# Optimization experiments

Hardware: AMD Instinct MI355X
Metric: run time of the kernel (lower is better)

The kernel has to match this reference:

```python
import jax, jax.numpy as jnp
import numpy as np
import math

N_HEADS = 16
EMBED = 1024
D_HEAD = EMBED // N_HEADS
B, L = 2, 2048


def setup_inputs() -> dict:
    key = jax.random.key(0)
    k1, k2, k3, k4, k5 = jax.random.split(key, 5)
    s = 0.02
    return {
        "x": jax.random.normal(k1, (B, L, EMBED), dtype=jnp.float32),
        "w_qkv": jax.random.normal(k2, (3 * EMBED, EMBED), dtype=jnp.float32) * s,
        "b_qkv": jax.random.normal(k3, (3 * EMBED,), dtype=jnp.float32) * s,
        "w_out": jax.random.normal(k4, (EMBED, EMBED), dtype=jnp.float32) * s,
        "b_out": jax.random.normal(k5, (EMBED,), dtype=jnp.float32) * s,
        "mask": 1,
    }


def reference(x, w_qkv, b_qkv, w_out, b_out, mask):
    b, l, e = x.shape
    qkv = x @ w_qkv.T + b_qkv                      # (B, L, 3E)
    q, k, v = jnp.split(qkv, 3, axis=-1)
    # (B, L, H, d) -> (B, H, L, d)
    q = q.reshape(b, l, N_HEADS, D_HEAD).transpose(0, 2, 1, 3)
    k = k.reshape(b, l, N_HEADS, D_HEAD).transpose(0, 2, 1, 3)
    v = v.reshape(b, l, N_HEADS, D_HEAD).transpose(0, 2, 1, 3)
    # NOTE: faithful to source bug -- scores use V, not K
    scores = jnp.einsum("bhld,bhmd->bhlm", q, v) * (1.0 / math.sqrt(D_HEAD))
    if mask:
        causal = jnp.triu(jnp.ones((l, l), dtype=bool), k=1)  # (L, L)
        scores = jnp.where(causal, -jnp.inf, scores)
    attn = jax.nn.softmax(scores, axis=-1)          # (B, H, L, L)
    out = jnp.einsum("bhlm,bhmd->bhld", attn, v)    # (B, H, L, d)
    # NOTE: faithful to source bug -- transpose(1,2) result discarded,
    # so reshape straight from (B, H, L, d) to (B, L, E)
    out = out.reshape(b, l, e)
    return out @ w_out.T + b_out
```

## Files before the change

kernel.cpp:

```cpp
#include <hip/hip_runtime.h>
#include <math.h>

constexpr int Lc = 2048, Ec = 1024, Hc = 16, Dc = 64;

typedef __attribute__((ext_vector_type(8))) short bf16x8;
typedef __attribute__((ext_vector_type(4))) float f32x4;
typedef unsigned short u16;
typedef unsigned int u32;

#define MFMA16(a, b, c) __builtin_amdgcn_mfma_f32_16x16x32_bf16(a, b, c, 0, 0, 0)

__device__ inline u16 f2bf(float f) {
  u32 u = __builtin_bit_cast(u32, f);
  u32 r = u + 0x7fff + ((u >> 16) & 1);
  return (u16)(r >> 16);
}

__device__ inline void gld16(const void* g, void* l) {
  __builtin_amdgcn_global_load_lds(
      (const __attribute__((address_space(1))) u32*)g,
      (__attribute__((address_space(3))) u32*)l, 16, 0, 0);
}

constexpr size_t XN = (size_t)4096 * 1024;
constexpr size_t WQN = (size_t)2048 * 1024;
constexpr size_t WON = (size_t)1024 * 1024;

__global__ __launch_bounds__(256) void convert_all(
    const float* __restrict__ x, const float* __restrict__ wqkv,
    const float* __restrict__ wout, u16* __restrict__ xb,
    u16* __restrict__ wqb, u16* __restrict__ wob)
{
  const size_t i = ((size_t)blockIdx.x * 256 + threadIdx.x) * 4;
  float4 v;
  u16* dst;
  if (i < XN) {
    v = *(const float4*)(x + i);
    dst = xb + i;
  } else if (i < XN + WQN) {
    const size_t off = i - XN;
    const size_t row = off >> 10, col = off & 1023;
    const size_t srow = row + ((row >> 10) << 10);
    v = *(const float4*)(wqkv + srow * 1024 + col);
    dst = wqb + off;
  } else {
    const size_t off = i - XN - WQN;
    v = *(const float4*)(wout + off);
    dst = wob + off;
  }
  u16 o0 = f2bf(v.x), o1 = f2bf(v.y), o2 = f2bf(v.z), o3 = f2bf(v.w);
  dst[0] = o0; dst[1] = o1; dst[2] = o2; dst[3] = o3;
}

__global__ __launch_bounds__(256) void gemm_qv(
    const u16* __restrict__ A, const u16* __restrict__ W,
    const float* __restrict__ bqkv, u16* __restrict__ Q, u16* __restrict__ V)
{
  __shared__ u16 As[128 * 32];
  __shared__ u16 Bs[128 * 32];
  const int tid = threadIdx.x;
  const int w = tid >> 6, lane = tid & 63;
  const int quad = lane >> 4, l16 = lane & 15;
  const int wm = w >> 1, wn = w & 1;
  const int rowTile = blockIdx.y * 128;
  const int colTile = blockIdx.x * 128;

  const int r0 = tid >> 2, o0 = (tid & 3) * 8;
  const u16* Ab0 = A + (size_t)(rowTile + r0) * 1024 + o0;
  const u16* Ab1 = A + (size_t)(rowTile + r0 + 64) * 1024 + o0;
  const u16* Bb0 = W + (size_t)(colTile + r0) * 1024 + o0;
  const u16* Bb1 = W + (size_t)(colTile + r0 + 64) * 1024 + o0;
  u16* lA0 = &As[(size_t)tid * 8];
  u16* lA1 = &As[(size_t)(tid + 256) * 8];
  u16* lB0 = &Bs[(size_t)tid * 8];
  u16* lB1 = &Bs[(size_t)(tid + 256) * 8];

  f32x4 acc[4][4] = {};

  for (int k0 = 0; k0 < 1024; k0 += 32) {
    __syncthreads();
    gld16(Ab0 + k0, lA0);
    gld16(Ab1 + k0, lA1);
    gld16(Bb0 + k0, lB0);
    gld16(Bb1 + k0, lB1);
    __syncthreads();
    bf16x8 af[4], bf[4];
#pragma unroll
    for (int s = 0; s < 4; ++s)
      af[s] = *(const bf16x8*)&As[(wm * 64 + s * 16 + l16) * 32 + quad * 8];
#pragma unroll
    for (int n = 0; n < 4; ++n)
      bf[n] = *(const bf16x8*)&Bs[(wn * 64 + n * 16 + l16) * 32 + quad * 8];
#pragma unroll
    for (int s = 0; s < 4; ++s)
#pragma unroll
      for (int n = 0; n < 4; ++n)
        acc[s][n] = MFMA16(af[s], bf[n], acc[s][n]);
  }

#pragma unroll
  for (int n = 0; n < 4; ++n) {
    const int gn = colTile + wn * 64 + n * 16 + l16;
    const bool isV = gn >= 1024;
    const float bias = bqkv[gn + (isV ? 1024 : 0)];
    const float scl = isV ? 1.0f : 0.125f;
    const int h = (gn & 1023) >> 6, d = gn & 63;
    u16* dst = isV ? V : Q;
#pragma unroll
    for (int s = 0; s < 4; ++s) {
#pragma unroll
      for (int r = 0; r < 4; ++r) {
        const int gm = rowTile + wm * 64 + s * 16 + quad * 4 + r;
        const int b = gm >> 11, l = gm & 2047;
        dst[(((size_t)(b * Hc + h)) * Lc + l) * Dc + d] = f2bf((acc[s][n][r] + bias) * scl);
      }
    }
  }
}

constexpr int VSTR = 72;
constexpr int VTSTR = 66;
constexpr int PSTR = 72;

__global__ __launch_bounds__(256) void attn_mfma(
    const u16* __restrict__ Q, const u16* __restrict__ V,
    u16* __restrict__ outA)
{
  __shared__ u16 Vs[64 * VSTR];
  __shared__ u16 VsT[64 * VTSTR];
  __shared__ u16 Ps[4][16 * PSTR];
  const int tid = threadIdx.x;
  const int w = tid >> 6, lane = tid & 63;
  const int quad = lane >> 4, l16 = lane & 15;
  const int bh = blockIdx.y;
  const int b = bh >> 4, h = bh & 15;
  const u16* Qb = Q + (size_t)bh * Lc * Dc;
  const u16* Vb = V + (size_t)bh * Lc * Dc;
  const int vr0 = tid >> 3, vd0 = (tid & 7) * 8;

  for (int half = 0; half < 2; ++half) {
    const int qt = half ? (31 - blockIdx.x) : blockIdx.x;
    const int q0 = qt * 64;
    const int nt = qt + 1;
    const int wqmin = q0 + w * 16;

    bf16x8 qf[2];
#pragma unroll
    for (int kk = 0; kk < 2; ++kk)
      qf[kk] = *(const bf16x8*)(Qb + (size_t)(q0 + w * 16 + l16) * 64 + kk * 32 + quad * 8);

    f32x4 O[4] = {};
    float lsum[4] = {0.f, 0.f, 0.f, 0.f};

    bf16x8 v0 = *(const bf16x8*)(Vb + (size_t)vr0 * 64 + vd0);
    bf16x8 v1 = *(const bf16x8*)(Vb + (size_t)(vr0 + 32) * 64 + vd0);

    for (int t = 0; t < nt; ++t) {
      const int kt = t * 64;
      __syncthreads();
      *(bf16x8*)&Vs[vr0 * VSTR + vd0] = v0;
      *(bf16x8*)&Vs[(vr0 + 32) * VSTR + vd0] = v1;
#pragma unroll
      for (int j = 0; j < 8; ++j) {
        VsT[(vd0 + j) * VTSTR + vr0] = (u16)v0[j];
        VsT[(vd0 + j) * VTSTR + vr0 + 32] = (u16)v1[j];
      }
      if (t + 1 < nt) {
        v0 = *(const bf16x8*)(Vb + (size_t)(kt + 64 + vr0) * 64 + vd0);
        v1 = *(const bf16x8*)(Vb + (size_t)(kt + 96 + vr0) * 64 + vd0);
      }
      __syncthreads();
      if (kt > wqmin + 15) continue;

      f32x4 sf[4] = {};
      bf16x8 bvf[2][4];
#pragma unroll
      for (int nb = 0; nb < 4; ++nb)
#pragma unroll
        for (int kk = 0; kk < 2; ++kk)
          bvf[kk][nb] = *(const bf16x8*)&Vs[(nb * 16 + l16) * VSTR + kk * 32 + quad * 8];
#pragma unroll
      for (int nb = 0; nb < 4; ++nb) {
        sf[nb] = MFMA16(qf[0], bvf[0][nb], sf[nb]);
        sf[nb] = MFMA16(qf[1], bvf[1][nb], sf[nb]);
      }

      const bool needmask = (kt + 63 > wqmin);
#pragma unroll
      for (int nb = 0; nb < 4; ++nb)
#pragma unroll
        for (int r = 0; r < 4; ++r) {
          float p = __expf(sf[nb][r]);
          if (needmask) {
            const int key = kt + nb * 16 + l16;
            const int qr = wqmin + quad * 4 + r;
            if (key > qr) p = 0.f;
          }
          lsum[r] += p;
          Ps[w][(quad * 4 + r) * PSTR + nb * 16 + l16] = f2bf(p);
        }

      bf16x8 pf[2];
#pragma unroll
      for (int kk = 0; kk < 2; ++kk)
        pf[kk] = *(const bf16x8*)&Ps[w][l16 * PSTR + kk * 32 + quad * 8];
#pragma unroll
      for (int db = 0; db < 4; ++db) {
        O[db] = MFMA16(pf[0], *(const bf16x8*)&VsT[(db * 16 + l16) * VTSTR + quad * 8], O[db]);
        O[db] = MFMA16(pf[1], *(const bf16x8*)&VsT[(db * 16 + l16) * VTSTR + 32 + quad * 8], O[db]);
      }
    }

#pragma unroll
    for (int r = 0; r < 4; ++r) {
      float l = lsum[r];
      l += __shfl_xor(l, 1);
      l += __shfl_xor(l, 2);
      l += __shfl_xor(l, 4);
      l += __shfl_xor(l, 8);
      const float inv = 1.f / l;
      const int q = q0 + w * 16 + quad * 4 + r;
      const int orow = h * 128 + (q >> 4);
      const int cbase = (q & 15) << 6;
#pragma unroll
      for (int db = 0; db < 4; ++db)
        outA[((size_t)b * Lc + orow) * Ec + cbase + db * 16 + l16] =
            f2bf(O[db][r] * inv);
    }
  }
}

__global__ __launch_bounds__(256) void gemm_out(
    const u16* __restrict__ A, const u16* __restrict__ W,
    const float* __restrict__ bias, float* __restrict__ out)
{
  __shared__ u16 As[128 * 32];
  __shared__ u16 Bs[128 * 32];
  const int tid = threadIdx.x;
  const int w = tid >> 6, lane = tid & 63;
  const int quad = lane >> 4, l16 = lane & 15;
  const int wm = w >> 1, wn = w & 1;
  const int rowTile = blockIdx.y * 128;
  const int colTile = blockIdx.x * 128;

  const int r0 = tid >> 2, o0 = (tid & 3) * 8;
  const u16* Ab0 = A + (size_t)(rowTile + r0) * 1024 + o0;
  const u16* Ab1 = A + (size_t)(rowTile + r0 + 64) * 1024 + o0;
  const u16* Bb0 = W + (size_t)(colTile + r0) * 1024 + o0;
  const u16* Bb1 = W + (size_t)(colTile + r0 + 64) * 1024 + o0;
  u16* lA0 = &As[(size_t)tid * 8];
  u16* lA1 = &As[(size_t)(tid + 256) * 8];
  u16* lB0 = &Bs[(size_t)tid * 8];
  u16* lB1 = &Bs[(size_t)(tid + 256) * 8];

  f32x4 acc[4][4] = {};

  for (int k0 = 0; k0 < 1024; k0 += 32) {
    __syncthreads();
    gld16(Ab0 + k0, lA0);
    gld16(Ab1 + k0, lA1);
    gld16(Bb0 + k0, lB0);
    gld16(Bb1 + k0, lB1);
    __syncthreads();
    bf16x8 af[4], bf[4];
#pragma unroll
    for (int s = 0; s < 4; ++s)
      af[s] = *(const bf16x8*)&As[(wm * 64 + s * 16 + l16) * 32 + quad * 8];
#pragma unroll
    for (int n = 0; n < 4; ++n)
      bf[n] = *(const bf16x8*)&Bs[(wn * 64 + n * 16 + l16) * 32 + quad * 8];
#pragma unroll
    for (int s = 0; s < 4; ++s)
#pragma unroll
      for (int n = 0; n < 4; ++n)
        acc[s][n] = MFMA16(af[s], bf[n], acc[s][n]);
  }

#pragma unroll
  for (int n = 0; n < 4; ++n) {
    const int gn = colTile + wn * 64 + n * 16 + l16;
    const float bn = bias[gn];
#pragma unroll
    for (int s = 0; s < 4; ++s)
#pragma unroll
      for (int r = 0; r < 4; ++r) {
        const int gm = rowTile + wm * 64 + s * 16 + quad * 4 + r;
        out[(size_t)gm * 1024 + gn] = acc[s][n][r] + bn;
      }
  }
}

extern "C" void kernel_launch(void* const* d_in, const int* in_sizes, int n_in,
                              void* d_out, int out_size, void* d_ws, size_t ws_size,
                              hipStream_t stream) {
  (void)in_sizes; (void)n_in; (void)out_size; (void)ws_size;
  const float* x     = (const float*)d_in[0];
  const float* w_qkv = (const float*)d_in[1];
  const float* b_qkv = (const float*)d_in[2];
  const float* w_out = (const float*)d_in[3];
  const float* b_out = (const float*)d_in[4];
  float* out = (float*)d_out;

  u16* xb  = (u16*)d_ws;
  u16* wqb = xb + XN;
  u16* wob = wqb + WQN;
  u16* Qw  = wob + WON;
  u16* Vw  = Qw + (size_t)2 * Hc * Lc * Dc;
  u16* Aw  = Vw + (size_t)2 * Hc * Lc * Dc;

  convert_all<<<7168, 256, 0, stream>>>(x, w_qkv, w_out, xb, wqb, wob);
  gemm_qv<<<dim3(16, 32), 256, 0, stream>>>(xb, wqb, b_qkv, Qw, Vw);
  attn_mfma<<<dim3(16, 32), 256, 0, stream>>>(Qw, Vw, Aw);
  gemm_out<<<dim3(8, 32), 256, 0, stream>>>(Aw, wob, b_out, out);
}
```

Baseline: 193.7 us.

## Double-buffer GEMM and attention LDS tiles with async loads, pre-transpose V

Both GEMMs now use two LDS buffers, so the next K tile is fetched with global_load_lds while the current one feeds the MFMAs. This also drops one barrier per iteration. A new kernel writes a transposed copy of V to the workspace, which lets the attention kernel load both V and V^T with async, XOR-swizzled direct-to-LDS loads in a double-buffered loop. That replaces the register staging and scattered per-element transpose stores. The cost is an extra kernel launch and a full extra read and write of V, plus more LDS per block. The attention loop also appears to rely on a single barrier per tile, so the correctness of the async-load ordering (no explicit vmcnt wait) is a risk.

```diff
diff --git a/kernel.cpp b/kernel.cpp
--- a/kernel.cpp
+++ b/kernel.cpp
@@ -52,12 +52,33 @@
   dst[0] = o0; dst[1] = o1; dst[2] = o2; dst[3] = o3;
 }
 
+__global__ __launch_bounds__(256) void transpose_v(
+    const u16* __restrict__ V, u16* __restrict__ Vt)
+{
+  __shared__ __align__(16) u16 T[64][72];
+  const int bh = blockIdx.y, lt = blockIdx.x * 64;
+  const int r = threadIdx.x >> 2;
+  const int c = (threadIdx.x & 3) * 16;
+  const u16* src = V + ((size_t)bh * Lc + lt) * Dc;
+  *(bf16x8*)&T[r][c]     = *(const bf16x8*)(src + (size_t)r * 64 + c);
+  *(bf16x8*)&T[r][c + 8] = *(const bf16x8*)(src + (size_t)r * 64 + c + 8);
+  __syncthreads();
+  bf16x8 o0, o1;
+#pragma unroll
+  for (int j = 0; j < 8; ++j) o0[j] = (short)T[c + j][r];
+#pragma unroll
+  for (int j = 0; j < 8; ++j) o1[j] = (short)T[c + 8 + j][r];
+  u16* dst = Vt + ((size_t)bh * Dc + r) * Lc + lt + c;
+  *(bf16x8*)dst = o0;
+  *(bf16x8*)(dst + 8) = o1;
+}
+
 __global__ __launch_bounds__(256) void gemm_qv(
     const u16* __restrict__ A, const u16* __restrict__ W,
     const float* __restrict__ bqkv, u16* __restrict__ Q, u16* __restrict__ V)
 {
-  __shared__ u16 As[128 * 32];
-  __shared__ u16 Bs[128 * 32];
+  __shared__ __align__(16) u16 As[2][4096];
+  __shared__ __align__(16) u16 Bs[2][4096];
   const int tid = threadIdx.x;
   const int w = tid >> 6, lane = tid & 63;
   const int quad = lane >> 4, l16 = lane & 15;
@@ -67,35 +88,40 @@
 
   const int r0 = tid >> 2, o0 = (tid & 3) * 8;
   const u16* Ab0 = A + (size_t)(rowTile + r0) * 1024 + o0;
-  const u16* Ab1 = A + (size_t)(rowTile + r0 + 64) * 1024 + o0;
+  const u16* Ab1 = Ab0 + (size_t)64 * 1024;
   const u16* Bb0 = W + (size_t)(colTile + r0) * 1024 + o0;
-  const u16* Bb1 = W + (size_t)(colTile + r0 + 64) * 1024 + o0;
-  u16* lA0 = &As[(size_t)tid * 8];
-  u16* lA1 = &As[(size_t)(tid + 256) * 8];
-  u16* lB0 = &Bs[(size_t)tid * 8];
-  u16* lB1 = &Bs[(size_t)(tid + 256) * 8];
+  const u16* Bb1 = Bb0 + (size_t)64 * 1024;
 
   f32x4 acc[4][4] = {};
 
+  gld16(Ab0, &As[0][tid * 8]);
+  gld16(Ab1, &As[0][2048 + tid * 8]);
+  gld16(Bb0, &Bs[0][tid * 8]);
+  gld16(Bb1, &Bs[0][2048 + tid * 8]);
+
+  int cur = 0;
   for (int k0 = 0; k0 < 1024; k0 += 32) {
     __syncthreads();
-    gld16(Ab0 + k0, lA0);
-    gld16(Ab1 + k0, lA1);
-    gld16(Bb0 + k0, lB0);
-    gld16(Bb1 + k0, lB1);
-    __syncthreads();
+    if (k0 + 32 < 1024) {
+      const int sb = cur ^ 1, kn = k0 + 32;
+      gld16(Ab0 + kn, &As[sb][tid * 8]);
+      gld16(Ab1 + kn, &As[sb][2048 + tid * 8]);
+      gld16(Bb0 + kn, &Bs[sb][tid * 8]);
+      gld16(Bb1 + kn, &Bs[sb][2048 + tid * 8]);
+    }
     bf16x8 af[4], bf[4];
 #pragma unroll
     for (int s = 0; s < 4; ++s)
-      af[s] = *(const bf16x8*)&As[(wm * 64 + s * 16 + l16) * 32 + quad * 8];
+      af[s] = *(const bf16x8*)&As[cur][(wm * 64 + s * 16 + l16) * 32 + quad * 8];
 #pragma unroll
     for (int n = 0; n < 4; ++n)
-      bf[n] = *(const bf16x8*)&Bs[(wn * 64 + n * 16 + l16) * 32 + quad * 8];
+      bf[n] = *(const bf16x8*)&Bs[cur][(wn * 64 + n * 16 + l16) * 32 + quad * 8];
 #pragma unroll
     for (int s = 0; s < 4; ++s)
 #pragma unroll
       for (int n = 0; n < 4; ++n)
         acc[s][n] = MFMA16(af[s], bf[n], acc[s][n]);
+    cur ^= 1;
   }
 
 #pragma unroll
@@ -118,17 +144,13 @@
   }
 }
 
-constexpr int VSTR = 72;
-constexpr int VTSTR = 66;
 constexpr int PSTR = 72;
 
 __global__ __launch_bounds__(256) void attn_mfma(
     const u16* __restrict__ Q, const u16* __restrict__ V,
-    u16* __restrict__ outA)
-{
-  __shared__ u16 Vs[64 * VSTR];
-  __shared__ u16 VsT[64 * VTSTR];
-  __shared__ u16 Ps[4][16 * PSTR];
+    const u16* __restrict__ Vt, u16* __restrict__ outA)
+{
+  __shared__ __align__(16) u16 lds[2 * 4096 + 2 * 4096 + 4 * 16 * PSTR];
   const int tid = threadIdx.x;
   const int w = tid >> 6, lane = tid & 63;
   const int quad = lane >> 4, l16 = lane & 15;
@@ -136,7 +158,25 @@
   const int b = bh >> 4, h = bh & 15;
   const u16* Qb = Q + (size_t)bh * Lc * Dc;
   const u16* Vb = V + (size_t)bh * Lc * Dc;
-  const int vr0 = tid >> 3, vd0 = (tid & 7) * 8;
+  const u16* Vtb = Vt + (size_t)bh * Dc * Lc;
+  u16* Ps = &lds[16384 + w * 16 * PSTR];
+
+  const int b1 = tid * 16, b2 = b1 + 4096;
+  const int e1 = (b1 ^ (((b1 >> 7) & 7) << 4)) >> 1;
+  const int e2 = (b2 ^ (((b2 >> 7) & 7) << 4)) >> 1;
+  const u16* vs1 = Vb + e1;
+  const u16* vs2 = Vb + e2;
+  const u16* ts1 = Vtb + (size_t)(e1 >> 6) * Lc + (e1 & 63);
+  const u16* ts2 = Vtb + (size_t)(e2 >> 6) * Lc + (e2 & 63);
+
+  int roff[4][2];
+#pragma unroll
+  for (int i = 0; i < 4; ++i)
+#pragma unroll
+    for (int kk = 0; kk < 2; ++kk) {
+      const int byte = ((i * 16 + l16) << 7) + kk * 64 + quad * 16;
+      roff[i][kk] = (byte ^ ((l16 & 7) << 4)) >> 1;
+    }
 
   for (int half = 0; half < 2; ++half) {
     const int qt = half ? (31 - blockIdx.x) : blockIdx.x;
@@ -152,63 +192,60 @@
     f32x4 O[4] = {};
     float lsum[4] = {0.f, 0.f, 0.f, 0.f};
 
-    bf16x8 v0 = *(const bf16x8*)(Vb + (size_t)vr0 * 64 + vd0);
-    bf16x8 v1 = *(const bf16x8*)(Vb + (size_t)(vr0 + 32) * 64 + vd0);
-
+    __syncthreads();
+    gld16(vs1, &lds[tid * 8]);
+    gld16(vs2, &lds[2048 + tid * 8]);
+    gld16(ts1, &lds[8192 + tid * 8]);
+    gld16(ts2, &lds[8192 + 2048 + tid * 8]);
+
+    int cur = 0;
     for (int t = 0; t < nt; ++t) {
       const int kt = t * 64;
       __syncthreads();
-      *(bf16x8*)&Vs[vr0 * VSTR + vd0] = v0;
-      *(bf16x8*)&Vs[(vr0 + 32) * VSTR + vd0] = v1;
-#pragma unroll
-      for (int j = 0; j < 8; ++j) {
-        VsT[(vd0 + j) * VTSTR + vr0] = (u16)v0[j];
-        VsT[(vd0 + j) * VTSTR + vr0 + 32] = (u16)v1[j];
+      if (t + 1 < nt) {
+        const int sb = cur ^ 1, nk = kt + 64;
+        gld16(vs1 + (size_t)nk * 64, &lds[sb * 4096 + tid * 8]);
+        gld16(vs2 + (size_t)nk * 64, &lds[sb * 4096 + 2048 + tid * 8]);
+        gld16(ts1 + nk, &lds[8192 + sb * 4096 + tid * 8]);
+        gld16(ts2 + nk, &lds[8192 + sb * 4096 + 2048 + tid * 8]);
       }
-      if (t + 1 < nt) {
-        v0 = *(const bf16x8*)(Vb + (size_t)(kt + 64 + vr0) * 64 + vd0);
-        v1 = *(const bf16x8*)(Vb + (size_t)(kt + 96 + vr0) * 64 + vd0);
+      if (kt <= wqmin + 15) {
+        const u16* VsB = &lds[cur * 4096];
+        const u16* VtB = &lds[8192 + cur * 4096];
+
+        f32x4 sf[4] = {};
+#pragma unroll
+        for (int nb = 0; nb < 4; ++nb) {
+          sf[nb] = MFMA16(qf[0], *(const bf16x8*)(VsB + roff[nb][0]), sf[nb]);
+          sf[nb] = MFMA16(qf[1], *(const bf16x8*)(VsB + roff[nb][1]), sf[nb]);
+        }
+
+        const bool needmask = (kt + 63 > wqmin);
+#pragma unroll
+        for (int nb = 0; nb < 4; ++nb)
+#pragma unroll
+          for (int r = 0; r < 4; ++r) {
+            float p = __expf(sf[nb][r]);
+            if (needmask) {
+              const int key = kt + nb * 16 + l16;
+              const int qr = wqmin + quad * 4 + r;
+              if (key > qr) p = 0.f;
+            }
+            lsum[r] += p;
+            Ps[(quad * 4 + r) * PSTR + nb * 16 + l16] = f2bf(p);
+          }
+
+        bf16x8 pf[2];
+#pragma unroll
+        for (int kk = 0; kk < 2; ++kk)
+          pf[kk] = *(const bf16x8*)&Ps[l16 * PSTR + kk * 32 + quad * 8];
+#pragma unroll
+        for (int db = 0; db < 4; ++db) {
+          O[db] = MFMA16(pf[0], *(const bf16x8*)(VtB + roff[db][0]), O[db]);
+          O[db] = MFMA16(pf[1], *(const bf16x8*)(VtB + roff[db][1]), O[db]);
+        }
       }
-      __syncthreads();
-      if (kt > wqmin + 15) continue;
-
-      f32x4 sf[4] = {};
-      bf16x8 bvf[2][4];
-#pragma unroll
-      for (int nb = 0; nb < 4; ++nb)
-#pragma unroll
-        for (int kk = 0; kk < 2; ++kk)
-          bvf[kk][nb] = *(const bf16x8*)&Vs[(nb * 16 + l16) * VSTR + kk * 32 + quad * 8];
-#pragma unroll
-      for (int nb = 0; nb < 4; ++nb) {
-        sf[nb] = MFMA16(qf[0], bvf[0][nb], sf[nb]);
-        sf[nb] = MFMA16(qf[1], bvf[1][nb], sf[nb]);
-      }
-
-      const bool needmask = (kt + 63 > wqmin);
-#pragma unroll
-      for (int nb = 0; nb < 4; ++nb)
-#pragma unroll
-        for (int r = 0; r < 4; ++r) {
-          float p = __expf(sf[nb][r]);
-          if (needmask) {
-            const int key = kt + nb * 16 + l16;
-            const int qr = wqmin + quad * 4 + r;
-            if (key > qr) p = 0.f;
-          }
-          lsum[r] += p;
-          Ps[w][(quad * 4 + r) * PSTR + nb * 16 + l16] = f2bf(p);
-        }
-
-      bf16x8 pf[2];
-#pragma unroll
-      for (int kk = 0; kk < 2; ++kk)
-        pf[kk] = *(const bf16x8*)&Ps[w][l16 * PSTR + kk * 32 + quad * 8];
-#pragma unroll
-      for (int db = 0; db < 4; ++db) {
-        O[db] = MFMA16(pf[0], *(const bf16x8*)&VsT[(db * 16 + l16) * VTSTR + quad * 8], O[db]);
-        O[db] = MFMA16(pf[1], *(const bf16x8*)&VsT[(db * 16 + l16) * VTSTR + 32 + quad * 8], O[db]);
-      }
+      cur ^= 1;
     }
 
 #pragma unroll
@@ -234,8 +271,8 @@
     const u16* __restrict__ A, const u16* __restrict__ W,
     const float* __restrict__ bias, float* __restrict__ out)
 {
-  __shared__ u16 As[128 * 32];
-  __shared__ u16 Bs[128 * 32];
+  __shared__ __align__(16) u16 As[2][4096];
+  __shared__ __align__(16) u16 Bs[2][4096];
   const int tid = threadIdx.x;
   const int w = tid >> 6, lane = tid & 63;
   const int quad = lane >> 4, l16 = lane & 15;
@@ -245,35 +282,40 @@
 
   const int r0 = tid >> 2, o0 = (tid & 3) * 8;
   const u16* Ab0 = A + (size_t)(rowTile + r0) * 1024 + o0;
-  const u16* Ab1 = A + (size_t)(rowTile + r0 + 64) * 1024 + o0;
+  const u16* Ab1 = Ab0 + (size_t)64 * 1024;
   const u16* Bb0 = W + (size_t)(colTile + r0) * 1024 + o0;
-  const u16* Bb1 = W + (size_t)(colTile + r0 + 64) * 1024 + o0;
-  u16* lA0 = &As[(size_t)tid * 8];
-  u16* lA1 = &As[(size_t)(tid + 256) * 8];
-  u16* lB0 = &Bs[(size_t)tid * 8];
-  u16* lB1 = &Bs[(size_t)(tid + 256) * 8];
+  const u16* Bb1 = Bb0 + (size_t)64 * 1024;
 
   f32x4 acc[4][4] = {};
 
+  gld16(Ab0, &As[0][tid * 8]);
+  gld16(Ab1, &As[0][2048 + tid * 8]);
+  gld16(Bb0, &Bs[0][tid * 8]);
+  gld16(Bb1, &Bs[0][2048 + tid * 8]);
+
+  int cur = 0;
   for (int k0 = 0; k0 < 1024; k0 += 32) {
     __syncthreads();
-    gld16(Ab0 + k0, lA0);
-    gld16(Ab1 + k0, lA1);
-    gld16(Bb0 + k0, lB0);
-    gld16(Bb1 + k0, lB1);
-    __syncthreads();
+    if (k0 + 32 < 1024) {
+      const int sb = cur ^ 1, kn = k0 + 32;
+      gld16(Ab0 + kn, &As[sb][tid * 8]);
+      gld16(Ab1 + kn, &As[sb][2048 + tid * 8]);
+      gld16(Bb0 + kn, &Bs[sb][tid * 8]);
+      gld16(Bb1 + kn, &Bs[sb][2048 + tid * 8]);
+    }
     bf16x8 af[4], bf[4];
 #pragma unroll
     for (int s = 0; s < 4; ++s)
-      af[s] = *(const bf16x8*)&As[(wm * 64 + s * 16 + l16) * 32 + quad * 8];
+      af[s] = *(const bf16x8*)&As[cur][(wm * 64 + s * 16 + l16) * 32 + quad * 8];
 #pragma unroll
     for (int n = 0; n < 4; ++n)
-      bf[n] = *(const bf16x8*)&Bs[(wn * 64 + n * 16 + l16) * 32 + quad * 8];
+      bf[n] = *(const bf16x8*)&Bs[cur][(wn * 64 + n * 16 + l16) * 32 + quad * 8];
 #pragma unroll
     for (int s = 0; s < 4; ++s)
 #pragma unroll
       for (int n = 0; n < 4; ++n)
         acc[s][n] = MFMA16(af[s], bf[n], acc[s][n]);
+    cur ^= 1;
   }
 
 #pragma unroll
@@ -306,10 +348,12 @@
   u16* wob = wqb + WQN;
   u16* Qw  = wob + WON;
   u16* Vw  = Qw + (size_t)2 * Hc * Lc * Dc;
-  u16* Aw  = Vw + (size_t)2 * Hc * Lc * Dc;
+  u16* Vtw = Vw + (size_t)2 * Hc * Lc * Dc;
+  u16* Aw  = Vtw + (size_t)2 * Hc * Lc * Dc;
 
   convert_all<<<7168, 256, 0, stream>>>(x, w_qkv, w_out, xb, wqb, wob);
   gemm_qv<<<dim3(16, 32), 256, 0, stream>>>(xb, wqb, b_qkv, Qw, Vw);
-  attn_mfma<<<dim3(16, 32), 256, 0, stream>>>(Qw, Vw, Aw);
+  transpose_v<<<dim3(32, 32), 256, 0, stream>>>(Vw, Vtw);
+  attn_mfma<<<dim3(16, 32), 256, 0, stream>>>(Qw, Vw, Vtw, Aw);
   gemm_out<<<dim3(8, 32), 256, 0, stream>>>(Aw, wob, b_out, out);
 }
```

Measured after the change: 179.8 us. -7.2%, faster.
